# Optimization experiments

Hardware: AMD Instinct MI355X
Metric: run time of the kernel (lower is better)

The kernel has to match this reference:

```python
import jax, jax.numpy as jnp
import numpy as np

Q = 10000   # num_question
D = 64      # dim_s
M = 50      # size_m
B = 64      # batch
T = 512     # seq_len


def setup_inputs() -> dict:
    key = jax.random.key(0)
    ks = jax.random.split(key, 14)
    s = 1.0 / np.sqrt(D)
    inp = {
        "question": jax.random.randint(ks[0], (B, T), 0, Q, dtype=jnp.int32),
        "response": jax.random.randint(ks[1], (B, T), 0, 2, dtype=jnp.int32),
        "mask": jnp.ones((B, T), dtype=jnp.float32),
        "k_emb": jax.random.normal(ks[2], (Q, D), jnp.float32) * s,
        "v_emb": jax.random.normal(ks[3], (2 * Q, D), jnp.float32) * s,
        "Mk": jax.random.normal(ks[4], (M, D), jnp.float32) * np.sqrt(2.0 / D),
        "Mv0": jax.random.normal(ks[5], (M, D), jnp.float32) * np.sqrt(2.0 / D),
        "e_W": jax.random.normal(ks[6], (D, D), jnp.float32) * s,
        "e_b": jnp.zeros((D,), jnp.float32),
        "a_W": jax.random.normal(ks[7], (D, D), jnp.float32) * s,
        "a_b": jnp.zeros((D,), jnp.float32),
        "f_W": jax.random.normal(ks[8], (2 * D, D), jnp.float32) * (1.0 / np.sqrt(2 * D)),
        "f_b": jnp.zeros((D,), jnp.float32),
        "p_W": jax.random.normal(ks[9], (D, 1), jnp.float32) * s,
        "p_b": jnp.zeros((1,), jnp.float32),
    }
    return inp


def reference(question, response, mask, k_emb, v_emb, Mk, Mv0,
              e_W, e_b, a_W, a_b, f_W, f_b, p_W, p_b):
    num_q = k_emb.shape[0]
    bsz = question.shape[0]
    x = question + num_q * response                      # [B,T] combined ids
    k = k_emb[question]                                  # [B,T,D]
    v = v_emb[x]                                         # [B,T,D]
    w = jax.nn.softmax(k @ Mk.T, axis=-1)                # [B,T,M] read/write weights
    e = jax.nn.sigmoid(v @ e_W + e_b)                    # [B,T,D] erase
    a = jnp.tanh(v @ a_W + a_b)                          # [B,T,D] add

    def step(Mvt, inp):
        wt, et, at, mt = inp                             # [B,M],[B,D],[B,D],[B]
        Mvn = Mvt * (1.0 - wt[:, :, None] * et[:, None, :]) + wt[:, :, None] * at[:, None, :]
        Mvt = jnp.where(mt[:, None, None] == 1, Mvn, Mvt)
        return Mvt, Mvt

    Mv0b = jnp.broadcast_to(Mv0, (bsz,) + Mv0.shape)     # [B,M,D]
    xs = (jnp.swapaxes(w, 0, 1), jnp.swapaxes(e, 0, 1),
          jnp.swapaxes(a, 0, 1), mask.T)
    _, Mv_seq = jax.lax.scan(step, Mv0b, xs)             # [T,B,M,D] states after steps 0..T-1
    # read at step t (t>=1) uses state after step t-1
    Mv_read = jnp.swapaxes(Mv_seq[:-1], 0, 1)            # [B,T-1,M,D]
    read = jnp.einsum('btm,btmd->btd', w[:, 1:], Mv_read)
    f = jnp.tanh(jnp.concatenate([read, k[:, 1:]], axis=-1) @ f_W + f_b)
    p = (f @ p_W + p_b).squeeze(-1)                      # [B,T-1]
    return p
```

## Files before the change

kernel.cpp:

```cpp
#include <hip/hip_runtime.h>
#include <cstddef>

#define QN 10000
#define DD 64
#define MM 50
#define BB 64
#define TT 512
#define WPAD 52
#define MG 25

#define PIN(arr, n)                                        \
  _Pragma("unroll") for (int _p = 0; _p < (n); ++_p)       \
      asm volatile("" : "+v"((arr)[_p]));

__global__ __launch_bounds__(256) void kPre(
    const int* __restrict__ question, const int* __restrict__ response,
    const float* __restrict__ mask,
    const float* __restrict__ k_emb, const float* __restrict__ v_emb,
    const float* __restrict__ Mk,
    const float* __restrict__ e_W, const float* __restrict__ e_b,
    const float* __restrict__ a_W, const float* __restrict__ a_b,
    float* __restrict__ w_buf, float* __restrict__ e_buf,
    float* __restrict__ a_buf) {
  const int lane = (int)(threadIdx.x & 63);
  const int wslot = __builtin_amdgcn_readfirstlane((int)(threadIdx.x >> 6));
  const int gw = blockIdx.x * 4 + wslot;
  const int NW = gridDim.x * 4;
  const int wq = (NW * 2) / 5;
  const int eq = (NW * 3) / 10;
  const int aq = NW - wq - eq;

  if (gw < wq) {
    const int idx = gw;
    const int stride4 = wq * 4;
    float mk[64];
    const int mrow = lane < MM ? lane : (MM - 1);
#pragma unroll
    for (int i = 0; i < 64; i += 4) {
      const float4 t4 = *(const float4*)(Mk + mrow * 64 + i);
      mk[i] = t4.x; mk[i + 1] = t4.y; mk[i + 2] = t4.z; mk[i + 3] = t4.w;
    }
    for (int base = idx * 4; base < BB * TT; base += stride4) {
      const int4 q4 = *(const int4*)(question + base);
      const float* __restrict__ kr0 = k_emb + (size_t)q4.x * 64;
      const float* __restrict__ kr1 = k_emb + (size_t)q4.y * 64;
      const float* __restrict__ kr2 = k_emb + (size_t)q4.z * 64;
      const float* __restrict__ kr3 = k_emb + (size_t)q4.w * 64;
      float l00=0.f,l01=0.f,l02=0.f,l03=0.f;
      float l10=0.f,l11=0.f,l12=0.f,l13=0.f;
      float l20=0.f,l21=0.f,l22=0.f,l23=0.f;
      float l30=0.f,l31=0.f,l32=0.f,l33=0.f;
#pragma unroll
      for (int i = 0; i < 64; i += 4) {
        const float4 k0 = *(const float4*)(kr0 + i);
        const float4 k1 = *(const float4*)(kr1 + i);
        const float4 k2 = *(const float4*)(kr2 + i);
        const float4 k3 = *(const float4*)(kr3 + i);
        l00 = fmaf(k0.x, mk[i], l00); l01 = fmaf(k0.y, mk[i+1], l01);
        l02 = fmaf(k0.z, mk[i+2], l02); l03 = fmaf(k0.w, mk[i+3], l03);
        l10 = fmaf(k1.x, mk[i], l10); l11 = fmaf(k1.y, mk[i+1], l11);
        l12 = fmaf(k1.z, mk[i+2], l12); l13 = fmaf(k1.w, mk[i+3], l13);
        l20 = fmaf(k2.x, mk[i], l20); l21 = fmaf(k2.y, mk[i+1], l21);
        l22 = fmaf(k2.z, mk[i+2], l22); l23 = fmaf(k2.w, mk[i+3], l23);
        l30 = fmaf(k3.x, mk[i], l30); l31 = fmaf(k3.y, mk[i+1], l31);
        l32 = fmaf(k3.z, mk[i+2], l32); l33 = fmaf(k3.w, mk[i+3], l33);
      }
      float lm[4];
      lm[0] = (l00 + l01) + (l02 + l03);
      lm[1] = (l10 + l11) + (l12 + l13);
      lm[2] = (l20 + l21) + (l22 + l23);
      lm[3] = (l30 + l31) + (l32 + l33);
#pragma unroll
      for (int r = 0; r < 4; ++r) {
        float lv = (lane < MM) ? lm[r] : -3.4e38f;
#pragma unroll
        for (int off = 32; off > 0; off >>= 1) lv = fmaxf(lv, __shfl_xor(lv, off));
        float pe = (lane < MM) ? __expf(lm[r] - lv) : 0.f;
        float ss = pe;
#pragma unroll
        for (int off = 32; off > 0; off >>= 1) ss += __shfl_xor(ss, off);
        if (lane < MM) w_buf[(size_t)(base + r) * WPAD + lane] = pe / ss;
      }
    }
  } else if (gw < wq + eq) {
    const int idx = gw - wq;
    const int stride4 = eq * 4;
    float ew[64];
#pragma unroll
    for (int i = 0; i < 64; ++i) ew[i] = e_W[i * 64 + lane];
    const float eb = e_b[lane];
    for (int base = idx * 4; base < BB * TT; base += stride4) {
      const int4 q4 = *(const int4*)(question + base);
      const int4 r4 = *(const int4*)(response + base);
      const float4 m4 = *(const float4*)(mask + base);
      const float* __restrict__ v0 = v_emb + ((size_t)q4.x + (size_t)QN * r4.x) * 64;
      const float* __restrict__ v1 = v_emb + ((size_t)q4.y + (size_t)QN * r4.y) * 64;
      const float* __restrict__ v2 = v_emb + ((size_t)q4.z + (size_t)QN * r4.z) * 64;
      const float* __restrict__ v3 = v_emb + ((size_t)q4.w + (size_t)QN * r4.w) * 64;
      float e00 = eb, e01 = 0.f, e10 = eb, e11 = 0.f;
      float e20 = eb, e21 = 0.f, e30 = eb, e31 = 0.f;
#pragma unroll
      for (int i = 0; i < 64; i += 4) {
        const float4 a0 = *(const float4*)(v0 + i);
        const float4 a1 = *(const float4*)(v1 + i);
        const float4 a2 = *(const float4*)(v2 + i);
        const float4 a3 = *(const float4*)(v3 + i);
        e00 = fmaf(a0.x, ew[i], e00);     e01 = fmaf(a0.y, ew[i + 1], e01);
        e00 = fmaf(a0.z, ew[i + 2], e00); e01 = fmaf(a0.w, ew[i + 3], e01);
        e10 = fmaf(a1.x, ew[i], e10);     e11 = fmaf(a1.y, ew[i + 1], e11);
        e10 = fmaf(a1.z, ew[i + 2], e10); e11 = fmaf(a1.w, ew[i + 3], e11);
        e20 = fmaf(a2.x, ew[i], e20);     e21 = fmaf(a2.y, ew[i + 1], e21);
        e20 = fmaf(a2.z, ew[i + 2], e20); e21 = fmaf(a2.w, ew[i + 3], e21);
        e30 = fmaf(a3.x, ew[i], e30);     e31 = fmaf(a3.y, ew[i + 1], e31);
        e30 = fmaf(a3.z, ew[i + 2], e30); e31 = fmaf(a3.w, ew[i + 3], e31);
      }
      const float mf0 = (m4.x == 1.0f) ? 1.0f : 0.0f;
      const float mf1 = (m4.y == 1.0f) ? 1.0f : 0.0f;
      const float mf2 = (m4.z == 1.0f) ? 1.0f : 0.0f;
      const float mf3 = (m4.w == 1.0f) ? 1.0f : 0.0f;
      e_buf[(size_t)(base + 0) * 64 + lane] = mf0 / (1.f + __expf(-(e00 + e01)));
      e_buf[(size_t)(base + 1) * 64 + lane] = mf1 / (1.f + __expf(-(e10 + e11)));
      e_buf[(size_t)(base + 2) * 64 + lane] = mf2 / (1.f + __expf(-(e20 + e21)));
      e_buf[(size_t)(base + 3) * 64 + lane] = mf3 / (1.f + __expf(-(e30 + e31)));
    }
  } else {
    const int idx = gw - wq - eq;
    const int stride4 = aq * 4;
    float aw[64];
#pragma unroll
    for (int i = 0; i < 64; ++i) aw[i] = a_W[i * 64 + lane];
    const float ab = a_b[lane];
    for (int base = idx * 4; base < BB * TT; base += stride4) {
      const int4 q4 = *(const int4*)(question + base);
      const int4 r4 = *(const int4*)(response + base);
      const float4 m4 = *(const float4*)(mask + base);
      const float* __restrict__ v0 = v_emb + ((size_t)q4.x + (size_t)QN * r4.x) * 64;
      const float* __restrict__ v1 = v_emb + ((size_t)q4.y + (size_t)QN * r4.y) * 64;
      const float* __restrict__ v2 = v_emb + ((size_t)q4.z + (size_t)QN * r4.z) * 64;
      const float* __restrict__ v3 = v_emb + ((size_t)q4.w + (size_t)QN * r4.w) * 64;
      float a00 = ab, a01 = 0.f, a10 = ab, a11 = 0.f;
      float a20 = ab, a21 = 0.f, a30 = ab, a31 = 0.f;
#pragma unroll
      for (int i = 0; i < 64; i += 4) {
        const float4 x0 = *(const float4*)(v0 + i);
        const float4 x1 = *(const float4*)(v1 + i);
        const float4 x2 = *(const float4*)(v2 + i);
        const float4 x3 = *(const float4*)(v3 + i);
        a00 = fmaf(x0.x, aw[i], a00);     a01 = fmaf(x0.y, aw[i + 1], a01);
        a00 = fmaf(x0.z, aw[i + 2], a00); a01 = fmaf(x0.w, aw[i + 3], a01);
        a10 = fmaf(x1.x, aw[i], a10);     a11 = fmaf(x1.y, aw[i + 1], a11);
        a10 = fmaf(x1.z, aw[i + 2], a10); a11 = fmaf(x1.w, aw[i + 3], a11);
        a20 = fmaf(x2.x, aw[i], a20);     a21 = fmaf(x2.y, aw[i + 1], a21);
        a20 = fmaf(x2.z, aw[i + 2], a20); a21 = fmaf(x2.w, aw[i + 3], a21);
        a30 = fmaf(x3.x, aw[i], a30);     a31 = fmaf(x3.y, aw[i + 1], a31);
        a30 = fmaf(x3.z, aw[i + 2], a30); a31 = fmaf(x3.w, aw[i + 3], a31);
      }
      const float mf0 = (m4.x == 1.0f) ? 1.0f : 0.0f;
      const float mf1 = (m4.y == 1.0f) ? 1.0f : 0.0f;
      const float mf2 = (m4.z == 1.0f) ? 1.0f : 0.0f;
      const float mf3 = (m4.w == 1.0f) ? 1.0f : 0.0f;
      const float s0 = a00 + a01, s1 = a10 + a11, s2 = a20 + a21, s3 = a30 + a31;
      a_buf[(size_t)(base + 0) * 64 + lane] = mf0 * (1.f - 2.f / (__expf(2.f * s0) + 1.f));
      a_buf[(size_t)(base + 1) * 64 + lane] = mf1 * (1.f - 2.f / (__expf(2.f * s1) + 1.f));
      a_buf[(size_t)(base + 2) * 64 + lane] = mf2 * (1.f - 2.f / (__expf(2.f * s2) + 1.f));
      a_buf[(size_t)(base + 3) * 64 + lane] = mf3 * (1.f - 2.f / (__expf(2.f * s3) + 1.f));
    }
  }
}

#define STAGE_W(wl_row, rowbase)                                            \
  {                                                                         \
    const float* __restrict__ wsrc = w_buf + (rowbase) * WPAD;              \
    _Pragma("unroll") for (int k = 0; k < 13; ++k) {                        \
      const int idx = lane + k * 64;                            \
      const int row = idx / 52;                                             \
      const int col = idx - row * 52;                                       \
      (wl_row)[row * 56 + col + (col >= 25 ? 3 : 0)] = wsrc[idx];           \
    }                                                                       \
  }

#define LOAD_WM(wm, wl_row, j, g)                                           \
  const float* __restrict__ wj_##j = (wl_row) + (j) * 56 + (g) * 28;        \
  const float4 q0_##j = *(const float4*)(wj_##j + 0);                       \
  const float4 q1_##j = *(const float4*)(wj_##j + 4);                       \
  const float4 q2_##j = *(const float4*)(wj_##j + 8);                       \
  const float4 q3_##j = *(const float4*)(wj_##j + 12);                      \
  const float4 q4_##j = *(const float4*)(wj_##j + 16);                      \
  const float4 q5_##j = *(const float4*)(wj_##j + 20);                      \
  const float4 q6_##j = *(const float4*)(wj_##j + 24);                      \
  const float wm[MG] = {q0_##j.x, q0_##j.y, q0_##j.z, q0_##j.w,             \
                        q1_##j.x, q1_##j.y, q1_##j.z, q1_##j.w,             \
                        q2_##j.x, q2_##j.y, q2_##j.z, q2_##j.w,             \
                        q3_##j.x, q3_##j.y, q3_##j.z, q3_##j.w,             \
                        q4_##j.x, q4_##j.y, q4_##j.z, q4_##j.w,             \
                        q5_##j.x, q5_##j.y, q5_##j.z, q5_##j.w, q6_##j.x};

__global__ __launch_bounds__(256) void kA16(
    const float* __restrict__ w_buf, const float* __restrict__ e_buf,
    const float* __restrict__ a_buf, float* __restrict__ AB) {
  __shared__ float wl[4][16 * 56];
  const int lane = (int)(threadIdx.x & 63);
  const int wslot = __builtin_amdgcn_readfirstlane((int)(threadIdx.x >> 6));
  const int u2 = blockIdx.x * 4 + wslot;
  if (u2 >= BB * 32 * 2) return;
  const int g = u2 & 1;
  const int unit = u2 >> 1;
  const int b = unit >> 5;
  const int c = unit & 31;
  const size_t rowbase = (size_t)b * TT + c * 16;
  const size_t eb0 = rowbase * 64 + lane;

  float ev[16], av[16];
#pragma unroll
  for (int j = 0; j < 16; ++j) {
    ev[j] = e_buf[eb0 + (size_t)j * 64];
    av[j] = a_buf[eb0 + (size_t)j * 64];
  }
  STAGE_W(wl[wslot], rowbase)

  float Am[MG], Bm[MG];
#pragma unroll
  for (int m = 0; m < MG; ++m) { Am[m] = 1.f; Bm[m] = 0.f; }

#pragma unroll
  for (int j = 0; j < 16; ++j) {
    LOAD_WM(wm, wl[wslot], j, g)
#pragma unroll
    for (int m = 0; m < MG; ++m) {
      const float al = fmaf(-wm[m], ev[j], 1.0f);
      const float be = wm[m] * av[j];
      Am[m] *= al;
      Bm[m] = fmaf(Bm[m], al, be);
    }
  }
  float* __restrict__ abp = AB + (size_t)unit * 6400 + (g * MG) * 128 + lane * 2;
#pragma unroll
  for (int m = 0; m < MG; ++m) {
    float2 o; o.x = Am[m]; o.y = Bm[m];
    *(float2*)(abp + m * 128) = o;
  }
}

__global__ __launch_bounds__(256) void kB_entry(
    const float* __restrict__ AB, const float* __restrict__ Mv0,
    float* __restrict__ entry, int C) {
  const int NT = gridDim.x * 256;
  for (int idx = blockIdx.x * 256 + (int)threadIdx.x; idx < BB * MM * 64;
       idx += NT) {
    const int b = idx / (MM * 64);
    const int r = idx - b * (MM * 64);
    float s = Mv0[r];
    const float* __restrict__ abp = AB + (size_t)b * C * 6400 + (size_t)r * 2;
    float* __restrict__ ep = entry + (size_t)b * C * 3200 + r;
    if (C == 32) {
      float2 ab[32];
#pragma unroll
      for (int c = 0; c < 32; ++c)
        ab[c] = *(const float2*)(abp + (size_t)c * 6400);
#pragma unroll
      for (int c = 0; c < 32; ++c) {
        ep[(size_t)c * 3200] = s;
        s = fmaf(ab[c].x, s, ab[c].y);
      }
    } else {
      float2 cur = *(const float2*)(abp);
      for (int c = 0; c < C; ++c) {
        ep[(size_t)c * 3200] = s;
        float2 nxt; nxt.x = 1.f; nxt.y = 0.f;
        if (c + 1 < C) nxt = *(const float2*)(abp + (size_t)(c + 1) * 6400);
        s = fmaf(cur.x, s, cur.y);
        cur = nxt;
      }
    }
  }
}

__global__ __launch_bounds__(256) void kCD2(
    const int* __restrict__ question,
    const float* __restrict__ w_buf, const float* __restrict__ e_buf,
    const float* __restrict__ a_buf, const float* __restrict__ entry,
    const float* __restrict__ k_emb,
    const float* __restrict__ f_W, const float* __restrict__ f_b,
    const float* __restrict__ p_W, const float* __restrict__ p_b,
    float* __restrict__ out) {
  __shared__ float wl[4][16 * 56];
  __shared__ float p_lds[4][16][64];
  __shared__ float pbuf[2][2][64];
  __shared__ float stg[4][64];
  const int lane = (int)(threadIdx.x & 63);
  const int wslot = __builtin_amdgcn_readfirstlane((int)(threadIdx.x >> 6));
  const int u2 = blockIdx.x * 4 + wslot;
  const int g = u2 & 1;
  const int unit = u2 >> 1;
  const int b = unit >> 5;
  const int c = unit & 31;
  const size_t rowbase = (size_t)b * TT + c * 16;
  const size_t eb0 = rowbase * 64 + lane;

  {
    float ev[16], av[16];
#pragma unroll
    for (int j = 0; j < 16; ++j) {
      ev[j] = e_buf[eb0 + (size_t)j * 64];
      av[j] = a_buf[eb0 + (size_t)j * 64];
    }
    float s[MG];
    const float* __restrict__ ep =
        entry + (size_t)unit * 3200 + (g * MG) * 64 + lane;
#pragma unroll
    for (int m = 0; m < MG; ++m) s[m] = ep[m * 64];
    STAGE_W(wl[wslot], rowbase)

#pragma unroll
    for (int j = 0; j < 16; ++j) {
      LOAD_WM(wm, wl[wslot], j, g)
      float a0 = 0.f, a1 = 0.f;
#pragma unroll
      for (int m = 0; m < MG - 1; m += 2) {
        a0 = fmaf(wm[m], s[m], a0);
        a1 = fmaf(wm[m + 1], s[m + 1], a1);
      }
      a0 = fmaf(wm[MG - 1], s[MG - 1], a0);
      p_lds[wslot][j][lane] = a0 + a1;
#pragma unroll
      for (int m = 0; m < MG; ++m)
        s[m] = fmaf(wm[m], fmaf(-s[m], ev[j], av[j]), s[m]);
    }
  }
  __syncthreads();

  const int p = wslot >> 1;
  const int uown = blockIdx.x * 2 + p;
  const int ob = uown >> 5;
  const int oc = uown & 31;
  const int t0 = oc * 16;

  float fw[64];
#pragma unroll
  for (int i = 0; i < 64; ++i) fw[i] = f_W[(g * 64 + i) * 64 + lane];
  PIN(fw, 64)
  const float fb = f_b[lane];
  const float pw = p_W[lane];
  const float pb = p_b[0];

  float nxt_k = 0.f;
  if (g == 1) {
    const int qn = question[(size_t)ob * TT + t0];
    nxt_k = k_emb[(size_t)qn * 64 + lane];
  }
  for (int j = 0; j < 16; ++j) {
    const int t = t0 + j;
    float cur;
    if (g == 0) {
      cur = p_lds[2 * p][j][lane] + p_lds[2 * p + 1][j][lane];
    } else {
      cur = nxt_k;
      if (j + 1 < 16) {
        const int qn = question[(size_t)ob * TT + t + 1];
        nxt_k = k_emb[(size_t)qn * 64 + lane];
      }
    }
    stg[wslot][lane] = cur;
    float f0 = (g == 0) ? fb : 0.f, f1 = 0.f, f2 = 0.f, f3 = 0.f;
#pragma unroll
    for (int i = 0; i < 64; i += 4) {
      const float4 xv = *(const float4*)&stg[wslot][i];
      f0 = fmaf(xv.x, fw[i], f0);
      f1 = fmaf(xv.y, fw[i + 1], f1);
      f2 = fmaf(xv.z, fw[i + 2], f2);
      f3 = fmaf(xv.w, fw[i + 3], f3);
    }
    const float partial = (f0 + f1) + (f2 + f3);
    const int pr = j & 1;
    if (g == 1) pbuf[pr][p][lane] = partial;
    __syncthreads();
    if (g == 0 && t >= 1) {
      const float f = partial + pbuf[pr][p][lane];
      const float t2 = __expf(2.f * f);
      const float fv = 1.f - 2.f / (t2 + 1.f);
      float acc = fv * pw;
#pragma unroll
      for (int off = 32; off > 0; off >>= 1) acc += __shfl_xor(acc, off);
      if (lane == 0) out[(size_t)ob * (TT - 1) + (t - 1)] = acc + pb;
    }
  }
}

__global__ __launch_bounds__(256) void kA_chunk(
    const float* __restrict__ w_buf, const float* __restrict__ e_buf,
    const float* __restrict__ a_buf, float* __restrict__ AB, int logC, int L) {
  const int lane = (int)(threadIdx.x & 63);
  const int wslot = __builtin_amdgcn_readfirstlane((int)(threadIdx.x >> 6));
  const int NW = gridDim.x * 4;
  const int C = 1 << logC;
  for (int u2 = blockIdx.x * 4 + wslot; u2 < BB * C * 2; u2 += NW) {
    const int g = u2 & 1;
    const int unit = u2 >> 1;
    const int b = unit >> logC;
    const int c = unit & (C - 1);
    float Am[MG], Bm[MG];
#pragma unroll
    for (int m = 0; m < MG; ++m) { Am[m] = 1.f; Bm[m] = 0.f; }
    const size_t rowbase = (size_t)b * TT + c * L;
#pragma unroll 2
    for (int j = 0; j < L; ++j) {
      const size_t row = rowbase + j;
      const float ed = e_buf[row * 64 + lane];
      const float ad = a_buf[row * 64 + lane];
      const float* __restrict__ wr = w_buf + row * WPAD + g * MG;
#pragma unroll
      for (int m = 0; m < MG; ++m) {
        const float wm = wr[m];
        const float al = fmaf(-wm, ed, 1.0f);
        const float be = wm * ad;
        Am[m] *= al;
        Bm[m] = fmaf(Bm[m], al, be);
      }
    }
    float* __restrict__ abp = AB + (size_t)unit * 6400 + (g * MG) * 128 + lane * 2;
#pragma unroll
    for (int m = 0; m < MG; ++m) {
      float2 o; o.x = Am[m]; o.y = Bm[m];
      *(float2*)(abp + m * 128) = o;
    }
  }
}

__global__ __launch_bounds__(256) void kC_read(
    const float* __restrict__ w_buf, const float* __restrict__ e_buf,
    const float* __restrict__ a_buf, const float* __restrict__ entry,
    const float* __restrict__ Mv0, float* __restrict__ read2,
    int logC, int L, int use_mv0) {
  const int lane = (int)(threadIdx.x & 63);
  const int wslot = __builtin_amdgcn_readfirstlane((int)(threadIdx.x >> 6));
  const int NW = gridDim.x * 4;
  const int C = 1 << logC;
  const size_t RN = (size_t)BB * (TT - 1) * 64;
  for (int u2 = blockIdx.x * 4 + wslot; u2 < BB * C * 2; u2 += NW) {
    const int g = u2 & 1;
    const int unit = u2 >> 1;
    const int b = unit >> logC;
    const int c = unit & (C - 1);
    float s[MG];
    if (use_mv0) {
#pragma unroll
      for (int m = 0; m < MG; ++m) s[m] = Mv0[(g * MG + m) * 64 + lane];
    } else {
      const float* __restrict__ ep =
          entry + (size_t)unit * 3200 + (g * MG) * 64 + lane;
#pragma unroll
      for (int m = 0; m < MG; ++m) s[m] = ep[m * 64];
    }
    const int t0 = c * L;
    float* __restrict__ rb = read2 + (size_t)g * RN;
    for (int j = 0; j < L; ++j) {
      const int t = t0 + j;
      const size_t row = (size_t)b * TT + t;
      const float ed = e_buf[row * 64 + lane];
      const float ad = a_buf[row * 64 + lane];
      const float* __restrict__ wr = w_buf + row * WPAD + g * MG;
      if (t >= 1) {
        float a0 = 0.f, a1 = 0.f;
#pragma unroll
        for (int m = 0; m < MG - 1; m += 2) {
          a0 = fmaf(wr[m], s[m], a0);
          a1 = fmaf(wr[m + 1], s[m + 1], a1);
        }
        a0 = fmaf(wr[MG - 1], s[MG - 1], a0);
        rb[((size_t)b * (TT - 1) + (t - 1)) * 64 + lane] = a0 + a1;
      }
#pragma unroll
      for (int m = 0; m < MG; ++m)
        s[m] = fmaf(wr[m], fmaf(-s[m], ed, ad), s[m]);
    }
  }
}

__global__ __launch_bounds__(256) void k3_out2(
    const int* __restrict__ question, const float* __restrict__ k_emb,
    const float* __restrict__ read2,
    const float* __restrict__ f_W, const float* __restrict__ f_b,
    const float* __restrict__ p_W, const float* __restrict__ p_b,
    float* __restrict__ out) {
  __shared__ float pbuf[2][2][64];
  __shared__ float stg[4][64];
  const int lane = (int)(threadIdx.x & 63);
  const int ws = __builtin_amdgcn_readfirstlane((int)(threadIdx.x >> 6));
  const int pair = ws >> 1;
  const int g = ws & 1;
  const int NP = gridDim.x * 2;
  const size_t RN = (size_t)BB * (TT - 1) * 64;
  const int R = BB * (TT - 1);
  const int iters = (R + NP - 1) / NP;

  float fw[64];
#pragma unroll
  for (int i = 0; i < 64; ++i) fw[i] = f_W[(g * 64 + i) * 64 + lane];
  PIN(fw, 64)
  const float fb = f_b[lane];
  const float pw = p_W[lane];
  const float pb = p_b[0];

  int row = blockIdx.x * 2 + pair;
  float cur = 0.f;
  if (row < R) {
    if (g == 0) {
      cur = read2[(size_t)row * 64 + lane] + read2[RN + (size_t)row * 64 + lane];
    } else {
      const int b = row / (TT - 1);
      const int tp = row - b * (TT - 1);
      const int qn = question[b * TT + tp + 1];
      cur = k_emb[(size_t)qn * 64 + lane];
    }
  }
  for (int it = 0; it < iters; ++it) {
    const int nrow = row + NP;
    float nxt = 0.f;
    if (nrow < R) {
      if (g == 0) {
        nxt = read2[(size_t)nrow * 64 + lane] +
              read2[RN + (size_t)nrow * 64 + lane];
      } else {
        const int nb = nrow / (TT - 1);
        const int ntp = nrow - nb * (TT - 1);
        const int nqn = question[nb * TT + ntp + 1];
        nxt = k_emb[(size_t)nqn * 64 + lane];
      }
    }
    const bool active = (row < R);
    float partial = 0.f;
    if (active) {
      stg[ws][lane] = cur;
      float f0 = (g == 0) ? fb : 0.f, f1 = 0.f, f2 = 0.f, f3 = 0.f;
#pragma unroll
      for (int i = 0; i < 64; i += 4) {
        const float4 xv = *(const float4*)&stg[ws][i];
        f0 = fmaf(xv.x, fw[i], f0);
        f1 = fmaf(xv.y, fw[i + 1], f1);
        f2 = fmaf(xv.z, fw[i + 2], f2);
        f3 = fmaf(xv.w, fw[i + 3], f3);
      }
      partial = (f0 + f1) + (f2 + f3);
    }
    const int pr = it & 1;
    if (active && g == 1) pbuf[pr][pair][lane] = partial;
    __syncthreads();
    if (active && g == 0) {
      const float f = partial + pbuf[pr][pair][lane];
      const float t2 = __expf(2.f * f);
      const float fv = 1.f - 2.f / (t2 + 1.f);
      float acc = fv * pw;
#pragma unroll
      for (int off = 32; off > 0; off >>= 1) acc += __shfl_xor(acc, off);
      if (lane == 0) out[row] = acc + pb;
    }
    row = nrow; cur = nxt;
  }
}

extern "C" void kernel_launch(void* const* d_in, const int* in_sizes, int n_in,
                              void* d_out, int out_size, void* d_ws, size_t ws_size,
                              hipStream_t stream) {
  const int*   question = (const int*)d_in[0];
  const int*   response = (const int*)d_in[1];
  const float* mask     = (const float*)d_in[2];
  const float* k_emb    = (const float*)d_in[3];
  const float* v_emb    = (const float*)d_in[4];
  const float* Mk       = (const float*)d_in[5];
  const float* Mv0      = (const float*)d_in[6];
  const float* e_W      = (const float*)d_in[7];
  const float* e_b      = (const float*)d_in[8];
  const float* a_W      = (const float*)d_in[9];
  const float* a_b      = (const float*)d_in[10];
  const float* f_W      = (const float*)d_in[11];
  const float* f_b      = (const float*)d_in[12];
  const float* p_W      = (const float*)d_in[13];
  const float* p_b      = (const float*)d_in[14];
  float* out = (float*)d_out;

  const size_t wN  = (size_t)BB * TT * WPAD;
  const size_t eN  = (size_t)BB * TT * 64;
  const size_t r2N = 2ull * BB * (TT - 1) * 64;
  float* ws = (float*)d_ws;
  float* w_buf  = ws;
  float* e_buf  = w_buf + wN;
  float* a_buf  = e_buf + eN;
  float* readws = a_buf + eN;
  float* AB_arr = readws + r2N;
  const size_t baseN = wN + 2 * eN + r2N;

  int C = 32, logC = 5;
  while (C >= 2) {
    const size_t need = (baseN + 9600ull * BB * C) * sizeof(float);
    if (need <= ws_size) break;
    C >>= 1; logC -= 1;
  }
  int useChunks = (C >= 2);
  if (!useChunks) { C = 1; logC = 0; }
  const int L = TT / C;
  float* entry = AB_arr + 6400ull * BB * C;

  hipLaunchKernelGGL(kPre, dim3(2048), dim3(256), 0, stream,
                     question, response, mask, k_emb, v_emb, Mk,
                     e_W, e_b, a_W, a_b, w_buf, e_buf, a_buf);

  if (C == 32) {
    hipLaunchKernelGGL(kA16, dim3(1024), dim3(256), 0, stream,
                       w_buf, e_buf, a_buf, AB_arr);
    hipLaunchKernelGGL(kB_entry, dim3((BB * MM * 64 + 255) / 256), dim3(256),
                       0, stream, AB_arr, Mv0, entry, C);
    hipLaunchKernelGGL(kCD2, dim3(1024), dim3(256), 0, stream,
                       question, w_buf, e_buf, a_buf, entry, k_emb,
                       f_W, f_b, p_W, p_b, out);
  } else {
    if (useChunks) {
      const int ublocksA = (BB * C * 2 + 3) / 4;
      hipLaunchKernelGGL(kA_chunk, dim3(ublocksA), dim3(256), 0, stream,
                         w_buf, e_buf, a_buf, AB_arr, logC, L);
      hipLaunchKernelGGL(kB_entry, dim3((BB * MM * 64 + 255) / 256), dim3(256),
                         0, stream, AB_arr, Mv0, entry, C);
    }
    const int ublocksC = (BB * C * 2 + 3) / 4;
    hipLaunchKernelGGL(kC_read, dim3(ublocksC), dim3(256), 0, stream,
                       w_buf, e_buf, a_buf, entry, Mv0, readws,
                       logC, L, useChunks ? 0 : 1);
    hipLaunchKernelGGL(k3_out2, dim3(1024), dim3(256), 0, stream,
                       question, k_emb, readws, f_W, f_b, p_W, p_b, out);
  }
}
```

Baseline: 173.2 us.

## Replace chunked affine-compose plus entry scan with direct sequential scan kernel

In the default 32-chunk path, the two-stage approach is dropped. It used to compute per-chunk affine coefficients (A,B) in one kernel and then scan them into chunk entry states in a second. A single kernel now walks all 512 timesteps per (b,m,d) element, recording the state at each chunk boundary. This removes one launch and the AB intermediate write and read. The cost is a fully serial 512-step dependency chain per thread across only 204800 threads, with strided global loads of w/e/a that are no longer reused through LDS.

```diff
diff --git a/kernel.cpp b/kernel.cpp
--- a/kernel.cpp
+++ b/kernel.cpp
@@ -168,6 +168,38 @@
   }
 }
 
+__global__ __launch_bounds__(256) void kScanE(
+    const float* __restrict__ w_buf, const float* __restrict__ e_buf,
+    const float* __restrict__ a_buf, const float* __restrict__ Mv0,
+    float* __restrict__ entry) {
+  const int idx = blockIdx.x * 256 + (int)threadIdx.x;
+  if (idx >= BB * MM * 64) return;
+  const int b = idx / (MM * 64);
+  const int r = idx - b * (MM * 64);
+  const int m = r >> 6;
+  const int d = r & 63;
+  float s = Mv0[r];
+  const float* __restrict__ wp  = w_buf + (size_t)b * TT * WPAD + m;
+  const float* __restrict__ ebp = e_buf + (size_t)b * TT * 64 + d;
+  const float* __restrict__ abp = a_buf + (size_t)b * TT * 64 + d;
+  float* __restrict__ ep = entry + (size_t)b * 32 * 3200 + r;
+
+  for (int c = 0; c < 32; ++c) {
+    ep[(size_t)c * 3200] = s;
+    const int t0 = c * 16;
+    float wv[16], evv[16], avv[16];
+#pragma unroll
+    for (int j = 0; j < 16; ++j) {
+      wv[j]  = wp[(size_t)(t0 + j) * WPAD];
+      evv[j] = ebp[(size_t)(t0 + j) * 64];
+      avv[j] = abp[(size_t)(t0 + j) * 64];
+    }
+#pragma unroll
+    for (int j = 0; j < 16; ++j)
+      s = fmaf(wv[j], fmaf(-s, evv[j], avv[j]), s);
+  }
+}
+
 #define STAGE_W(wl_row, rowbase)                                            \
   {                                                                         \
     const float* __restrict__ wsrc = w_buf + (rowbase) * WPAD;              \
@@ -194,86 +226,6 @@
                         q3_##j.x, q3_##j.y, q3_##j.z, q3_##j.w,             \
                         q4_##j.x, q4_##j.y, q4_##j.z, q4_##j.w,             \
                         q5_##j.x, q5_##j.y, q5_##j.z, q5_##j.w, q6_##j.x};
-
-__global__ __launch_bounds__(256) void kA16(
-    const float* __restrict__ w_buf, const float* __restrict__ e_buf,
-    const float* __restrict__ a_buf, float* __restrict__ AB) {
-  __shared__ float wl[4][16 * 56];
-  const int lane = (int)(threadIdx.x & 63);
-  const int wslot = __builtin_amdgcn_readfirstlane((int)(threadIdx.x >> 6));
-  const int u2 = blockIdx.x * 4 + wslot;
-  if (u2 >= BB * 32 * 2) return;
-  const int g = u2 & 1;
-  const int unit = u2 >> 1;
-  const int b = unit >> 5;
-  const int c = unit & 31;
-  const size_t rowbase = (size_t)b * TT + c * 16;
-  const size_t eb0 = rowbase * 64 + lane;
-
-  float ev[16], av[16];
-#pragma unroll
-  for (int j = 0; j < 16; ++j) {
-    ev[j] = e_buf[eb0 + (size_t)j * 64];
-    av[j] = a_buf[eb0 + (size_t)j * 64];
-  }
-  STAGE_W(wl[wslot], rowbase)
-
-  float Am[MG], Bm[MG];
-#pragma unroll
-  for (int m = 0; m < MG; ++m) { Am[m] = 1.f; Bm[m] = 0.f; }
-
-#pragma unroll
-  for (int j = 0; j < 16; ++j) {
-    LOAD_WM(wm, wl[wslot], j, g)
-#pragma unroll
-    for (int m = 0; m < MG; ++m) {
-      const float al = fmaf(-wm[m], ev[j], 1.0f);
-      const float be = wm[m] * av[j];
-      Am[m] *= al;
-      Bm[m] = fmaf(Bm[m], al, be);
-    }
-  }
-  float* __restrict__ abp = AB + (size_t)unit * 6400 + (g * MG) * 128 + lane * 2;
-#pragma unroll
-  for (int m = 0; m < MG; ++m) {
-    float2 o; o.x = Am[m]; o.y = Bm[m];
-    *(float2*)(abp + m * 128) = o;
-  }
-}
-
-__global__ __launch_bounds__(256) void kB_entry(
-    const float* __restrict__ AB, const float* __restrict__ Mv0,
-    float* __restrict__ entry, int C) {
-  const int NT = gridDim.x * 256;
-  for (int idx = blockIdx.x * 256 + (int)threadIdx.x; idx < BB * MM * 64;
-       idx += NT) {
-    const int b = idx / (MM * 64);
-    const int r = idx - b * (MM * 64);
-    float s = Mv0[r];
-    const float* __restrict__ abp = AB + (size_t)b * C * 6400 + (size_t)r * 2;
-    float* __restrict__ ep = entry + (size_t)b * C * 3200 + r;
-    if (C == 32) {
-      float2 ab[32];
-#pragma unroll
-      for (int c = 0; c < 32; ++c)
-        ab[c] = *(const float2*)(abp + (size_t)c * 6400);
-#pragma unroll
-      for (int c = 0; c < 32; ++c) {
-        ep[(size_t)c * 3200] = s;
-        s = fmaf(ab[c].x, s, ab[c].y);
-      }
-    } else {
-      float2 cur = *(const float2*)(abp);
-      for (int c = 0; c < C; ++c) {
-        ep[(size_t)c * 3200] = s;
-        float2 nxt; nxt.x = 1.f; nxt.y = 0.f;
-        if (c + 1 < C) nxt = *(const float2*)(abp + (size_t)(c + 1) * 6400);
-        s = fmaf(cur.x, s, cur.y);
-        cur = nxt;
-      }
-    }
-  }
-}
 
 __global__ __launch_bounds__(256) void kCD2(
     const int* __restrict__ question,
@@ -426,6 +378,28 @@
   }
 }
 
+__global__ __launch_bounds__(256) void kB_entry(
+    const float* __restrict__ AB, const float* __restrict__ Mv0,
+    float* __restrict__ entry, int C) {
+  const int NT = gridDim.x * 256;
+  for (int idx = blockIdx.x * 256 + (int)threadIdx.x; idx < BB * MM * 64;
+       idx += NT) {
+    const int b = idx / (MM * 64);
+    const int r = idx - b * (MM * 64);
+    float s = Mv0[r];
+    const float* __restrict__ abp = AB + (size_t)b * C * 6400 + (size_t)r * 2;
+    float* __restrict__ ep = entry + (size_t)b * C * 3200 + r;
+    float2 cur = *(const float2*)(abp);
+    for (int c = 0; c < C; ++c) {
+      ep[(size_t)c * 3200] = s;
+      float2 nxt; nxt.x = 1.f; nxt.y = 0.f;
+      if (c + 1 < C) nxt = *(const float2*)(abp + (size_t)(c + 1) * 6400);
+      s = fmaf(cur.x, s, cur.y);
+      cur = nxt;
+    }
+  }
+}
+
 __global__ __launch_bounds__(256) void kC_read(
     const float* __restrict__ w_buf, const float* __restrict__ e_buf,
     const float* __restrict__ a_buf, const float* __restrict__ entry,
@@ -605,10 +579,8 @@
                      e_W, e_b, a_W, a_b, w_buf, e_buf, a_buf);
 
   if (C == 32) {
-    hipLaunchKernelGGL(kA16, dim3(1024), dim3(256), 0, stream,
-                       w_buf, e_buf, a_buf, AB_arr);
-    hipLaunchKernelGGL(kB_entry, dim3((BB * MM * 64 + 255) / 256), dim3(256),
-                       0, stream, AB_arr, Mv0, entry, C);
+    hipLaunchKernelGGL(kScanE, dim3((BB * MM * 64) / 256), dim3(256), 0,
+                       stream, w_buf, e_buf, a_buf, Mv0, entry);
     hipLaunchKernelGGL(kCD2, dim3(1024), dim3(256), 0, stream,
                        question, w_buf, e_buf, a_buf, entry, k_emb,
                        f_W, f_b, p_W, p_b, out);
```

New measurement: 194.4 us. 12.3% more time.
